# Kernel tuning notes

Measured on AMD Instinct MI355X. Metric: run time of the kernel, lower is better.

The kernel has to match this reference:

```python
import jax, jax.numpy as jnp
import numpy as np

D_MODEL = 1024
NUM_HEADS = 16
D_K = 1024
D_V = 1024
D_IN = 1024
THETA = 10000.0
B, S = 2, 2048


def setup_inputs() -> dict:
    key = jax.random.key(0)
    k1, k2, k3, k4, k5 = jax.random.split(key, 5)
    std_qkv = (2.0 / (D_IN + D_K)) ** 0.5
    std_o = (2.0 / (D_V + D_MODEL)) ** 0.5
    x = jax.random.normal(k1, (B, S, D_IN), jnp.float32)
    wq = jax.random.normal(k2, (D_IN, D_K), jnp.float32) * std_qkv
    wk = jax.random.normal(k3, (D_IN, D_K), jnp.float32) * std_qkv
    wv = jax.random.normal(k4, (D_IN, D_V), jnp.float32) * std_qkv
    wo = jax.random.normal(k5, (D_V, D_MODEL), jnp.float32) * std_o
    return {"x": x, "wq": wq, "wk": wk, "wv": wv, "wo": wo}


def _rope(t, theta):
    # t: (H, B, S, hd) -- interleaved-pair RoPE, angles pos * theta^(-2i/hd)
    hd = t.shape[-1]
    inv_freq = 1.0 / (theta ** (jnp.arange(0, hd, 2, dtype=jnp.float32) / hd))  # (hd/2,)
    pos = jnp.arange(t.shape[-2], dtype=jnp.float32)
    ang = pos[:, None] * inv_freq[None, :]                                       # (S, hd/2)
    cos, sin = jnp.cos(ang), jnp.sin(ang)
    tp = t.reshape(t.shape[:-1] + (hd // 2, 2))
    t0, t1 = tp[..., 0], tp[..., 1]
    out = jnp.stack([t0 * cos - t1 * sin, t0 * sin + t1 * cos], axis=-1)
    return out.reshape(t.shape)


def reference(x, wq, wk, wv, wo):
    b, s, _ = x.shape
    hd = D_K // NUM_HEADS
    hdv = D_V // NUM_HEADS
    # fused QKV proj (math identical to concat-then-matmul)
    q = jnp.einsum('bsd,de->bse', x, wq).reshape(b, s, NUM_HEADS, hd).transpose(2, 0, 1, 3)
    k = jnp.einsum('bsd,de->bse', x, wk).reshape(b, s, NUM_HEADS, hd).transpose(2, 0, 1, 3)
    v = jnp.einsum('bsd,de->bse', x, wv).reshape(b, s, NUM_HEADS, hdv).transpose(2, 0, 1, 3)
    q = _rope(q, THETA)
    k = _rope(k, THETA)
    scale = 1.0 / jnp.sqrt(jnp.asarray(hd, jnp.float32))
    scores = jnp.einsum('hbqd,hbkd->hbqk', q, k) * scale                 # (H,B,S,S)
    causal = jnp.tril(jnp.ones((s, s), dtype=bool))
    scores = jnp.where(causal, scores, -jnp.inf)
    attn = jax.nn.softmax(scores, axis=-1)
    o = jnp.einsum('hbqk,hbkd->hbqd', attn, v)                            # (H,B,S,hdv)
    o = o.transpose(1, 2, 0, 3).reshape(b, s, D_V)                        # merge heads (outer)
    return jnp.einsum('bsd,de->bse', o, wo)
```

## Files before the change

kernel.cpp:

```cpp
#include <hip/hip_runtime.h>
#include <stdint.h>

typedef __attribute__((ext_vector_type(8))) short short8;
typedef __attribute__((ext_vector_type(4))) float f32x4;
typedef __attribute__((ext_vector_type(16))) float f32x16;
typedef __attribute__((ext_vector_type(4))) unsigned short ushort4v;
typedef __attribute__((ext_vector_type(2))) unsigned int uint2v;

static __device__ __forceinline__ unsigned short f2b(float f) {
  union { float f; unsigned int u; } v; v.f = f;
  unsigned int r = v.u + 0x7FFFu + ((v.u >> 16) & 1u);
  return (unsigned short)(r >> 16);
}

static __device__ __forceinline__ float exp2fast(float x) {
#if __has_builtin(__builtin_amdgcn_exp2f)
  return __builtin_amdgcn_exp2f(x);
#else
  return exp2f(x);
#endif
}

static __device__ __forceinline__ unsigned int cvtpk(float lo, float hi) {
  unsigned int r;
  asm("v_cvt_pk_bf16_f32 %0, %1, %2" : "=v"(r) : "v"(lo), "v"(hi));
  return r;
}

static __device__ __forceinline__ float xor32max(float x) {
#if __has_builtin(__builtin_amdgcn_permlane32_swap)
  unsigned u = __float_as_uint(x);
  uint2v r = __builtin_amdgcn_permlane32_swap(u, u, false, false);
  return fmaxf(__uint_as_float(r[0]), __uint_as_float(r[1]));
#else
  return fmaxf(x, __shfl_xor(x, 32));
#endif
}
static __device__ __forceinline__ float xor32add(float x) {
#if __has_builtin(__builtin_amdgcn_permlane32_swap)
  unsigned u = __float_as_uint(x);
  uint2v r = __builtin_amdgcn_permlane32_swap(u, u, false, false);
  return __uint_as_float(r[0]) + __uint_as_float(r[1]);
#else
  return x + __shfl_xor(x, 32);
#endif
}

static __device__ __forceinline__ void gload16(const void* g, void* l) {
  __builtin_amdgcn_global_load_lds(
      (const __attribute__((address_space(1))) unsigned int*)g,
      (__attribute__((address_space(3))) unsigned int*)l, 16, 0, 0);
}


__global__ __launch_bounds__(256) void prep_kernel(
    const float* __restrict__ x, const float* __restrict__ wq,
    const float* __restrict__ wk, const float* __restrict__ wv,
    const float* __restrict__ wo, unsigned short* __restrict__ xb,
    unsigned short* __restrict__ wT, float* __restrict__ ct,
    float* __restrict__ st) {
  __shared__ float t[32][33];
  const int bid = blockIdx.x, tid = threadIdx.x;
  if (bid < 4096) {
    int i = (bid * 256 + tid) * 4;
    float4 v = *(const float4*)(x + i);
    ushort4v o = { f2b(v.x), f2b(v.y), f2b(v.z), f2b(v.w) };
    *(ushort4v*)(xb + i) = o;
  } else if (bid < 8192) {
    int tt = bid - 4096;
    int z = tt >> 10, xy = tt & 1023;
    const float* src = (z == 0) ? wq : (z == 1) ? wk : (z == 2) ? wv : wo;
    unsigned short* dst = wT + (size_t)z * 1048576;
    int tx = tid & 31, ty = tid >> 5;
    int n0 = (xy & 31) * 32, k0 = (xy >> 5) * 32;
#pragma unroll
    for (int i = 0; i < 4; ++i) {
      int r = ty + i * 8;
      t[r][tx] = src[(size_t)(k0 + r) * 1024 + n0 + tx];
    }
    __syncthreads();
#pragma unroll
    for (int i = 0; i < 4; ++i) {
      int r = ty + i * 8;
      dst[(size_t)(n0 + r) * 1024 + k0 + tx] = f2b(t[tx][r]);
    }
  } else {
    int i = (bid - 8192) * 256 + tid;
    int s = i >> 5, p = i & 31;
    float ang = (float)s * powf(10000.0f, -(float)(2 * p) / 64.0f);
    ct[i] = cosf(ang);
    st[i] = sinf(ang);
  }
}


__global__ __launch_bounds__(256) void gemm_kernel(
    const unsigned short* __restrict__ A, const unsigned short* __restrict__ WT,
    unsigned short* __restrict__ Qb, unsigned short* __restrict__ Kb,
    unsigned short* __restrict__ VTb,
    const float* __restrict__ ctab, const float* __restrict__ stab) {
  __shared__ unsigned short As[128 * 32];
  __shared__ unsigned short Bs[128 * 32];
  const int tid = threadIdx.x;
  const int w = tid >> 6, lane = tid & 63;
  const int m0 = blockIdx.x * 128, n0 = blockIdx.y * 128;
  const int mode = blockIdx.z;
  const unsigned short* Bt = WT + (size_t)mode * 1048576;
  const int wr = w >> 1, wc = w & 1;
  const int srow = lane >> 2, scol = lane & 3;
  f32x4 acc[4][4] = {};
  for (int k0 = 0; k0 < 1024; k0 += 32) {
#pragma unroll
    for (int c = 0; c < 2; ++c) {
      int chunk = w * 2 + c;
      gload16(A + (size_t)(m0 + chunk * 16 + srow) * 1024 + k0 + scol * 8,
              (char*)As + chunk * 1024);
      gload16(Bt + (size_t)(n0 + chunk * 16 + srow) * 1024 + k0 + scol * 8,
              (char*)Bs + chunk * 1024);
    }
    __syncthreads();
    short8 af[4], bf[4];
#pragma unroll
    for (int i = 0; i < 4; ++i) {
      af[i] = *(const short8*)((const char*)As +
              ((wr * 64 + i * 16 + (lane & 15)) * 64 + (lane >> 4) * 16));
      bf[i] = *(const short8*)((const char*)Bs +
              ((wc * 64 + i * 16 + (lane & 15)) * 64 + (lane >> 4) * 16));
    }
#pragma unroll
    for (int i = 0; i < 4; ++i)
#pragma unroll
      for (int j = 0; j < 4; ++j)
        acc[i][j] = __builtin_amdgcn_mfma_f32_16x16x32_bf16(af[i], bf[j], acc[i][j], 0, 0, 0);
    __syncthreads();
  }

  if (mode < 2) {
    unsigned short* dst = mode ? Kb : Qb;
    const float qscale = mode ? 1.0f : 0.125f * 1.44269504088896f;
#pragma unroll
    for (int i = 0; i < 4; ++i) {
#pragma unroll
      for (int j = 0; j < 4; ++j) {
        int n = n0 + wc * 64 + j * 16 + (lane & 15);
        int h = n >> 6, d = n & 63;
        int pairIdx = d >> 1;
        bool even = (n & 1) == 0;
#pragma unroll
        for (int r = 0; r < 4; ++r) {
          int m = m0 + wr * 64 + i * 16 + (lane >> 4) * 4 + r;
          int b = m >> 11, s = m & 2047;
          float v = acc[i][j][r];
          float pv = __shfl_xor(v, 1);
          float c = ctab[s * 32 + pairIdx], sn = stab[s * 32 + pairIdx];
          float ov = (even ? (v * c - pv * sn) : (pv * sn + v * c)) * qscale;
          dst[(size_t)((h * 2 + b) * 2048 + s) * 64 + d] = f2b(ov);
        }
      }
    }
  } else {
#pragma unroll
    for (int i = 0; i < 4; ++i) {
#pragma unroll
      for (int j = 0; j < 4; ++j) {
        int n = n0 + wc * 64 + j * 16 + (lane & 15);
        int h = n >> 6, d = n & 63;
        int mBase = m0 + wr * 64 + i * 16 + (lane >> 4) * 4;
        int b = mBase >> 11, s = mBase & 2047;
        ushort4v pk = { f2b(acc[i][j][0]), f2b(acc[i][j][1]),
                        f2b(acc[i][j][2]), f2b(acc[i][j][3]) };
        *(ushort4v*)(VTb + (size_t)((h * 2 + b) * 64 + d) * 2048 + s) = pk;
      }
    }
  }
}


__global__ __launch_bounds__(128) void gemm_final_kernel(
    const unsigned short* __restrict__ A, const unsigned short* __restrict__ Bt,
    float* __restrict__ Fout) {
  __shared__ unsigned short As[64 * 32];
  __shared__ unsigned short Bs[128 * 32];
  const int tid = threadIdx.x;
  const int w = tid >> 6, lane = tid & 63;
  const int m0 = blockIdx.x * 64, n0 = blockIdx.y * 128;
  const int srow = lane >> 2, scol = lane & 3;
  f32x4 acc[4][4] = {};
  for (int k0 = 0; k0 < 1024; k0 += 32) {
#pragma unroll
    for (int c = 0; c < 2; ++c) {
      int chunk = w * 2 + c;
      gload16(A + (size_t)(m0 + chunk * 16 + srow) * 1024 + k0 + scol * 8,
              (char*)As + chunk * 1024);
    }
#pragma unroll
    for (int c = 0; c < 4; ++c) {
      int chunk = w * 4 + c;
      gload16(Bt + (size_t)(n0 + chunk * 16 + srow) * 1024 + k0 + scol * 8,
              (char*)Bs + chunk * 1024);
    }
    __syncthreads();
    short8 af[4], bf[4];
#pragma unroll
    for (int i = 0; i < 4; ++i) {
      af[i] = *(const short8*)((const char*)As +
              ((i * 16 + (lane & 15)) * 64 + (lane >> 4) * 16));
      bf[i] = *(const short8*)((const char*)Bs +
              ((w * 64 + i * 16 + (lane & 15)) * 64 + (lane >> 4) * 16));
    }
#pragma unroll
    for (int i = 0; i < 4; ++i)
#pragma unroll
      for (int j = 0; j < 4; ++j)
        acc[i][j] = __builtin_amdgcn_mfma_f32_16x16x32_bf16(af[i], bf[j], acc[i][j], 0, 0, 0);
    __syncthreads();
  }
#pragma unroll
  for (int i = 0; i < 4; ++i)
#pragma unroll
    for (int j = 0; j < 4; ++j) {
      int n = n0 + w * 64 + j * 16 + (lane & 15);
#pragma unroll
      for (int r = 0; r < 4; ++r) {
        int m = m0 + i * 16 + (lane >> 4) * 4 + r;
        Fout[(size_t)m * 1024 + n] = acc[i][j][r];
      }
    }
}


__global__ __launch_bounds__(256) void attn_kernel(
    const unsigned short* __restrict__ Qb, const unsigned short* __restrict__ Kb,
    const unsigned short* __restrict__ VTb, unsigned short* __restrict__ Ob) {
  __shared__ unsigned short Ks[2][64 * 64];
  __shared__ unsigned short Vs[2][64 * 64];
  const int tid = threadIdx.x, w = tid >> 6, lane = tid & 63;
  const int lq = lane & 31, hi = lane >> 5;
  const int hb = blockIdx.y;
  const int bxx = blockIdx.x ^ ((hb >> 4) << 3);
  const int qt = (bxx < 8) ? bxx : 23 - bxx;
  const int h = hb >> 1, b = hb & 1;
  const unsigned short* Qhb = Qb + (size_t)hb * 2048 * 64;
  const unsigned short* Khb = Kb + (size_t)hb * 2048 * 64;
  const unsigned short* Vhb = VTb + (size_t)hb * 64 * 2048;
  const int qbase = qt * 128 + w * 32;
  const int swq = (lq & 7) << 4;
  const int ktmax = 2 * qt + 1;

  short8 qf[4];
#pragma unroll
  for (int s = 0; s < 4; ++s)
    qf[s] = *(const short8*)(Qhb + (size_t)(qbase + lq) * 64 + s * 16 + hi * 8);

  const f32x16 Z16 = {0,0,0,0,0,0,0,0,0,0,0,0,0,0,0,0};
  f32x16 o0 = Z16, o1 = Z16;
  float m = -__builtin_inff(), ls = 0.f;

  const int r0 = tid >> 3, f0 = tid & 7;
  const int so0 = r0 * 128 + ((f0 * 16) ^ ((r0 & 7) << 4));
  short8 gK[2], gV[2];
  gK[0] = *(const short8*)(Khb + (size_t)r0 * 64 + f0 * 8);
  gK[1] = *(const short8*)(Khb + (size_t)(r0 + 32) * 64 + f0 * 8);
  gV[0] = *(const short8*)(Vhb + (size_t)r0 * 2048 + f0 * 8);
  gV[1] = *(const short8*)(Vhb + (size_t)(r0 + 32) * 2048 + f0 * 8);
  *(short8*)((char*)Ks[0] + so0) = gK[0];
  *(short8*)((char*)Ks[0] + so0 + 32 * 128) = gK[1];
  *(short8*)((char*)Vs[0] + so0) = gV[0];
  *(short8*)((char*)Vs[0] + so0 + 32 * 128) = gV[1];
  __syncthreads();

  for (int kt = 0; kt <= ktmax; ++kt) {
    const int cur = kt & 1;
    if (kt < ktmax) {
      int kk0 = (kt + 1) * 64;
      gK[0] = *(const short8*)(Khb + (size_t)(kk0 + r0) * 64 + f0 * 8);
      gK[1] = *(const short8*)(Khb + (size_t)(kk0 + r0 + 32) * 64 + f0 * 8);
      gV[0] = *(const short8*)(Vhb + (size_t)r0 * 2048 + kk0 + f0 * 8);
      gV[1] = *(const short8*)(Vhb + (size_t)(r0 + 32) * 2048 + kk0 + f0 * 8);
    }
    if (kt * 64 <= qbase + 31) {
      const unsigned short* Ksb = Ks[cur];
      const unsigned short* Vsb = Vs[cur];
      f32x16 s0 = Z16, s1 = Z16;
      __builtin_amdgcn_s_setprio(1);
#pragma unroll
      for (int st = 0; st < 4; ++st) {
        short8 a0 = *(const short8*)((const char*)Ksb + lq * 128 +
                    ((st * 32 + hi * 16) ^ swq));
        short8 a1 = *(const short8*)((const char*)Ksb + (32 + lq) * 128 +
                    ((st * 32 + hi * 16) ^ swq));
        s0 = __builtin_amdgcn_mfma_f32_32x32x16_bf16(a0, qf[st], s0, 0, 0, 0);
        s1 = __builtin_amdgcn_mfma_f32_32x32x16_bf16(a1, qf[st], s1, 0, 0, 0);
      }
      __builtin_amdgcn_s_setprio(0);

      if (kt * 64 + 63 > qbase) {
        int relk = qbase + lq - kt * 64;
#pragma unroll
        for (int r = 0; r < 16; ++r) {
          int km = (r & 3) + 8 * (r >> 2) + 4 * hi;
          if (km > relk) s0[r] = -__builtin_inff();
          if (km + 32 > relk) s1[r] = -__builtin_inff();
        }
      }

      float t8[8];
#pragma unroll
      for (int r = 0; r < 8; ++r)
        t8[r] = fmaxf(fmaxf(s0[2 * r], s0[2 * r + 1]),
                      fmaxf(s1[2 * r], s1[2 * r + 1]));
      float mA = fmaxf(fmaxf(t8[0], t8[1]), fmaxf(t8[2], t8[3]));
      float mB = fmaxf(fmaxf(t8[4], t8[5]), fmaxf(t8[6], t8[7]));
      float mx = xor32max(fmaxf(mA, mB));

      if (__any(mx > m + 8.0f)) {
        float nm = fmaxf(m, mx);
        float al = exp2fast(m - nm);
        m = nm;
        ls *= al;
        o0 *= al;
        o1 *= al;
      }
      float ps0 = 0.f, ps1 = 0.f, ps2 = 0.f, ps3 = 0.f;
#pragma unroll
      for (int r = 0; r < 16; ++r) {
        float p = exp2fast(s0[r] - m);
        s0[r] = p;
        if (r < 8) ps0 += p; else ps1 += p;
      }
#pragma unroll
      for (int r = 0; r < 16; ++r) {
        float p = exp2fast(s1[r] - m);
        s1[r] = p;
        if (r < 8) ps2 += p; else ps3 += p;
      }
      ls += (ps0 + ps1) + (ps2 + ps3);

      unsigned int pk0[8], pk1[8];
#pragma unroll
      for (int jp = 0; jp < 8; ++jp) {
        pk0[jp] = cvtpk(s0[2 * jp], s0[2 * jp + 1]);
        pk1[jp] = cvtpk(s1[2 * jp], s1[2 * jp + 1]);
      }
      __builtin_amdgcn_s_setprio(1);
#pragma unroll
      for (int ks = 0; ks < 4; ++ks) {
        const int off = 4 * (ks & 1);
        unsigned int a0 = (ks < 2) ? pk0[off + 0] : pk1[off + 0];
        unsigned int a1 = (ks < 2) ? pk0[off + 1] : pk1[off + 1];
        unsigned int b0 = (ks < 2) ? pk0[off + 2] : pk1[off + 2];
        unsigned int b1 = (ks < 2) ? pk0[off + 3] : pk1[off + 3];
        uint2v w0 = __builtin_amdgcn_permlane32_swap(a0, b0, false, false);
        uint2v w1 = __builtin_amdgcn_permlane32_swap(a1, b1, false, false);
        union { unsigned int u[4]; short8 s; } F;
        F.u[0] = w0[0]; F.u[1] = w1[0]; F.u[2] = w0[1]; F.u[3] = w1[1];
        short8 v0 = *(const short8*)((const char*)Vsb + lq * 128 +
                    ((ks * 32 + hi * 16) ^ swq));
        short8 v1 = *(const short8*)((const char*)Vsb + (32 + lq) * 128 +
                    ((ks * 32 + hi * 16) ^ swq));
        o0 = __builtin_amdgcn_mfma_f32_32x32x16_bf16(v0, F.s, o0, 0, 0, 0);
        o1 = __builtin_amdgcn_mfma_f32_32x32x16_bf16(v1, F.s, o1, 0, 0, 0);
      }
      __builtin_amdgcn_s_setprio(0);
    }
    if (kt < ktmax) {
      *(short8*)((char*)Ks[cur ^ 1] + so0) = gK[0];
      *(short8*)((char*)Ks[cur ^ 1] + so0 + 32 * 128) = gK[1];
      *(short8*)((char*)Vs[cur ^ 1] + so0) = gV[0];
      *(short8*)((char*)Vs[cur ^ 1] + so0 + 32 * 128) = gV[1];
    }
    __syncthreads();
  }

  ls = xor32add(ls);
  float invl = 1.0f / ls;
  char* Osw = (char*)Ks + w * 4096;
#pragma unroll
  for (int jp = 0; jp < 8; ++jp) {
    const int r = 2 * jp;
    const int km = (r & 3) + 8 * (r >> 2) + 4 * hi;
    unsigned int pa = cvtpk(o0[r] * invl, o0[r + 1] * invl);
    unsigned int pb = cvtpk(o1[r] * invl, o1[r + 1] * invl);
    *(unsigned int*)(Osw + lq * 128 + ((2 * km) ^ swq)) = pa;
    *(unsigned int*)(Osw + lq * 128 + ((2 * (km + 32)) ^ swq)) = pb;
  }
  __builtin_amdgcn_wave_barrier();
#pragma unroll
  for (int pass = 0; pass < 4; ++pass) {
    int q2 = pass * 8 + (lane >> 3);
    int c16 = (lane & 7) * 16;
    short8 vrow = *(const short8*)(Osw + q2 * 128 + (c16 ^ ((q2 & 7) << 4)));
    int srow = qbase + q2;
    *(short8*)(Ob + (size_t)(b * 2048 + srow) * 1024 + h * 64 + (lane & 7) * 8) = vrow;
  }
}


extern "C" void kernel_launch(void* const* d_in, const int* in_sizes, int n_in,
                              void* d_out, int out_size, void* d_ws, size_t ws_size,
                              hipStream_t stream) {
  const float* x  = (const float*)d_in[0];
  const float* wq = (const float*)d_in[1];
  const float* wk = (const float*)d_in[2];
  const float* wv = (const float*)d_in[3];
  const float* wo = (const float*)d_in[4];
  float* out = (float*)d_out;

  char* ws = (char*)d_ws;
  const size_t SZ = 8388608;
  unsigned short* xb  = (unsigned short*)(ws);
  unsigned short* wT  = (unsigned short*)(ws + SZ);
  unsigned short* Qb  = (unsigned short*)(ws + 2 * SZ);
  unsigned short* Kb  = (unsigned short*)(ws + 3 * SZ);
  unsigned short* VTb = (unsigned short*)(ws + 4 * SZ);
  unsigned short* Ob  = (unsigned short*)(ws + 5 * SZ);
  float* ctab = (float*)(ws + 6 * SZ);
  float* stab = (float*)(ws + 6 * SZ + 262144);
  if (ws_size < 6 * SZ + 2 * 262144) return;

  prep_kernel<<<8448, 256, 0, stream>>>(x, wq, wk, wv, wo, xb, wT, ctab, stab);
  gemm_kernel<<<dim3(32, 8, 3), 256, 0, stream>>>(xb, wT, Qb, Kb, VTb, ctab, stab);
  attn_kernel<<<dim3(16, 32), 256, 0, stream>>>(Qb, Kb, VTb, Ob);
  gemm_final_kernel<<<dim3(64, 8), 128, 0, stream>>>(Ob, wT + 3 * 1048576, out);
}
```

Measured before the change: 135.4 us.

## Split attention KV range in two halves with a separate combine kernel

Each query tile's causal key range is split into two halves handled by separate blocks, doubling the attention grid to 1024 blocks. The unnormalised partial outputs and per-row max and sum statistics go to workspace, and a new combine kernel merges them log-sum-exp style into the bf16 head-merged output. The aim is better occupancy and load balance on the many-CU device, with launch bounds requesting 4 blocks per CU. The cost is an extra kernel launch, extra global traffic for the partials, and extra bf16 rounding of the unnormalised partials before the merge.

```diff
diff --git a/kernel.cpp b/kernel.cpp
--- a/kernel.cpp
+++ b/kernel.cpp
@@ -229,23 +229,26 @@
 }
 
 
-__global__ __launch_bounds__(256) void attn_kernel(
+__global__ __launch_bounds__(256, 4) void attn_kernel(
     const unsigned short* __restrict__ Qb, const unsigned short* __restrict__ Kb,
-    const unsigned short* __restrict__ VTb, unsigned short* __restrict__ Ob) {
+    const unsigned short* __restrict__ VTb, unsigned short* __restrict__ P0,
+    unsigned short* __restrict__ P1, float* __restrict__ mls) {
   __shared__ unsigned short Ks[2][64 * 64];
   __shared__ unsigned short Vs[2][64 * 64];
   const int tid = threadIdx.x, w = tid >> 6, lane = tid & 63;
   const int lq = lane & 31, hi = lane >> 5;
   const int hb = blockIdx.y;
-  const int bxx = blockIdx.x ^ ((hb >> 4) << 3);
-  const int qt = (bxx < 8) ? bxx : 23 - bxx;
+  const int half = blockIdx.x >> 4;
+  const int i4 = blockIdx.x & 15;
+  const int qt = (i4 < 8) ? i4 : 23 - i4;
   const int h = hb >> 1, b = hb & 1;
   const unsigned short* Qhb = Qb + (size_t)hb * 2048 * 64;
   const unsigned short* Khb = Kb + (size_t)hb * 2048 * 64;
   const unsigned short* Vhb = VTb + (size_t)hb * 64 * 2048;
   const int qbase = qt * 128 + w * 32;
   const int swq = (lq & 7) << 4;
-  const int ktmax = 2 * qt + 1;
+  const int kt0 = half ? (qt + 1) : 0;
+  const int ktend = half ? (2 * qt + 2) : (qt + 1);
 
   short8 qf[4];
 #pragma unroll
@@ -259,19 +262,22 @@
   const int r0 = tid >> 3, f0 = tid & 7;
   const int so0 = r0 * 128 + ((f0 * 16) ^ ((r0 & 7) << 4));
   short8 gK[2], gV[2];
-  gK[0] = *(const short8*)(Khb + (size_t)r0 * 64 + f0 * 8);
-  gK[1] = *(const short8*)(Khb + (size_t)(r0 + 32) * 64 + f0 * 8);
-  gV[0] = *(const short8*)(Vhb + (size_t)r0 * 2048 + f0 * 8);
-  gV[1] = *(const short8*)(Vhb + (size_t)(r0 + 32) * 2048 + f0 * 8);
+  {
+    int kk0 = kt0 * 64;
+    gK[0] = *(const short8*)(Khb + (size_t)(kk0 + r0) * 64 + f0 * 8);
+    gK[1] = *(const short8*)(Khb + (size_t)(kk0 + r0 + 32) * 64 + f0 * 8);
+    gV[0] = *(const short8*)(Vhb + (size_t)r0 * 2048 + kk0 + f0 * 8);
+    gV[1] = *(const short8*)(Vhb + (size_t)(r0 + 32) * 2048 + kk0 + f0 * 8);
+  }
   *(short8*)((char*)Ks[0] + so0) = gK[0];
   *(short8*)((char*)Ks[0] + so0 + 32 * 128) = gK[1];
   *(short8*)((char*)Vs[0] + so0) = gV[0];
   *(short8*)((char*)Vs[0] + so0 + 32 * 128) = gV[1];
   __syncthreads();
 
-  for (int kt = 0; kt <= ktmax; ++kt) {
-    const int cur = kt & 1;
-    if (kt < ktmax) {
+  for (int kt = kt0; kt < ktend; ++kt) {
+    const int cur = (kt - kt0) & 1;
+    if (kt + 1 < ktend) {
       int kk0 = (kt + 1) * 64;
       gK[0] = *(const short8*)(Khb + (size_t)(kk0 + r0) * 64 + f0 * 8);
       gK[1] = *(const short8*)(Khb + (size_t)(kk0 + r0 + 32) * 64 + f0 * 8);
@@ -363,7 +369,7 @@
       }
       __builtin_amdgcn_s_setprio(0);
     }
-    if (kt < ktmax) {
+    if (kt + 1 < ktend) {
       *(short8*)((char*)Ks[cur ^ 1] + so0) = gK[0];
       *(short8*)((char*)Ks[cur ^ 1] + so0 + 32 * 128) = gK[1];
       *(short8*)((char*)Vs[cur ^ 1] + so0) = gV[0];
@@ -373,14 +379,19 @@
   }
 
   ls = xor32add(ls);
-  float invl = 1.0f / ls;
+  if (hi == 0) {
+    float* mlsJ = mls + (size_t)(((half * 32 + hb) * 16 + qt) * 2) * 128;
+    mlsJ[w * 32 + lq] = m;
+    mlsJ[128 + w * 32 + lq] = ls;
+  }
+  unsigned short* P = (half ? P1 : P0) + (size_t)(hb * 16 + qt) * 128 * 64;
   char* Osw = (char*)Ks + w * 4096;
 #pragma unroll
   for (int jp = 0; jp < 8; ++jp) {
     const int r = 2 * jp;
     const int km = (r & 3) + 8 * (r >> 2) + 4 * hi;
-    unsigned int pa = cvtpk(o0[r] * invl, o0[r + 1] * invl);
-    unsigned int pb = cvtpk(o1[r] * invl, o1[r + 1] * invl);
+    unsigned int pa = cvtpk(o0[r], o0[r + 1]);
+    unsigned int pb = cvtpk(o1[r], o1[r + 1]);
     *(unsigned int*)(Osw + lq * 128 + ((2 * km) ^ swq)) = pa;
     *(unsigned int*)(Osw + lq * 128 + ((2 * (km + 32)) ^ swq)) = pb;
   }
@@ -390,8 +401,40 @@
     int q2 = pass * 8 + (lane >> 3);
     int c16 = (lane & 7) * 16;
     short8 vrow = *(const short8*)(Osw + q2 * 128 + (c16 ^ ((q2 & 7) << 4)));
-    int srow = qbase + q2;
-    *(short8*)(Ob + (size_t)(b * 2048 + srow) * 1024 + h * 64 + (lane & 7) * 8) = vrow;
+    *(short8*)(P + (size_t)(w * 32 + q2) * 64 + (lane & 7) * 8) = vrow;
+  }
+}
+
+
+__global__ __launch_bounds__(256) void combine_kernel(
+    const unsigned short* __restrict__ P0, const unsigned short* __restrict__ P1,
+    const float* __restrict__ mls, unsigned short* __restrict__ Obf) {
+  const int qt = blockIdx.x, hb = blockIdx.y;
+  const int t = threadIdx.x;
+  const int q = t >> 1, dh = (t & 1) * 32;
+  const float* m0p = mls + (size_t)(((0 * 32 + hb) * 16 + qt) * 2) * 128;
+  const float* m1p = mls + (size_t)(((1 * 32 + hb) * 16 + qt) * 2) * 128;
+  float m0 = m0p[q], ls0 = m0p[128 + q];
+  float m1 = m1p[q], ls1 = m1p[128 + q];
+  float M = fmaxf(m0, m1);
+  float w0 = exp2fast(m0 - M), w1 = exp2fast(m1 - M);
+  float inv = 1.0f / (ls0 * w0 + ls1 * w1);
+  float f0 = w0 * inv, f1 = w1 * inv;
+  size_t rowoff = ((size_t)(hb * 16 + qt) * 128 + q) * 64 + dh;
+  int b = hb & 1, h = hb >> 1;
+  unsigned short* dst = Obf + ((size_t)(b * 2048 + qt * 128 + q)) * 1024 + h * 64 + dh;
+#pragma unroll
+  for (int c = 0; c < 32; c += 8) {
+    union { short8 s; unsigned short u[8]; } a, bb, o;
+    a.s = *(const short8*)(P0 + rowoff + c);
+    bb.s = *(const short8*)(P1 + rowoff + c);
+#pragma unroll
+    for (int e = 0; e < 8; ++e) {
+      float p0 = __uint_as_float((unsigned)a.u[e] << 16);
+      float p1 = __uint_as_float((unsigned)bb.u[e] << 16);
+      o.u[e] = f2b(p0 * f0 + p1 * f1);
+    }
+    *(short8*)(dst + c) = o.s;
   }
 }
 
@@ -413,13 +456,18 @@
   unsigned short* Qb  = (unsigned short*)(ws + 2 * SZ);
   unsigned short* Kb  = (unsigned short*)(ws + 3 * SZ);
   unsigned short* VTb = (unsigned short*)(ws + 4 * SZ);
-  unsigned short* Ob  = (unsigned short*)(ws + 5 * SZ);
+  unsigned short* P0  = (unsigned short*)(ws + 5 * SZ);
   float* ctab = (float*)(ws + 6 * SZ);
-  float* stab = (float*)(ws + 6 * SZ + 262144);
-  if (ws_size < 6 * SZ + 2 * 262144) return;
+  float* stab = ctab + 65536;
+  float* mls  = ctab;
+  if (ws_size < 6 * SZ + 1048576) return;
+
+  unsigned short* P1  = xb;
+  unsigned short* Obf = Qb;
 
   prep_kernel<<<8448, 256, 0, stream>>>(x, wq, wk, wv, wo, xb, wT, ctab, stab);
   gemm_kernel<<<dim3(32, 8, 3), 256, 0, stream>>>(xb, wT, Qb, Kb, VTb, ctab, stab);
-  attn_kernel<<<dim3(16, 32), 256, 0, stream>>>(Qb, Kb, VTb, Ob);
-  gemm_final_kernel<<<dim3(64, 8), 128, 0, stream>>>(Ob, wT + 3 * 1048576, out);
-}
+  attn_kernel<<<dim3(32, 32), 256, 0, stream>>>(Qb, Kb, VTb, P0, P1, mls);
+  combine_kernel<<<dim3(16, 32), 256, 0, stream>>>(P0, P1, mls, Obf);
+  gemm_final_kernel<<<dim3(64, 8), 128, 0, stream>>>(Obf, wT + 3 * 1048576, out);
+}
```

Result: slower. 143.7 us (+6.1%).
